# Kernel tuning notes

Measured on AMD Instinct MI355X. Metric: run time of the kernel, lower is better.

Reference implementation:

```python
import jax, jax.numpy as jnp
import numpy as np
from jax.ops import segment_sum

N_NODES = 500_000
N_EDGES = 16_000_000


def gcn_conv(x, W, b, src, dst, n_nodes):
    """PyG GCNConv: linear transform, add self-loops, sym deg norm, scatter-add."""
    xw = x @ W  # [N, out]
    # degree including self-loop (edge weight 1 each)
    deg = segment_sum(jnp.ones((src.shape[0],), xw.dtype), dst, num_segments=n_nodes) + 1.0
    dinv = jax.lax.rsqrt(deg)  # deg^{-1/2}, deg >= 1 so safe
    norm = dinv[src] * dinv[dst]  # [E]
    msg = xw[src] * norm[:, None]  # [E, out]
    agg = segment_sum(msg, dst, num_segments=n_nodes)
    # self-loop contribution: norm_ii = dinv_i^2
    agg = agg + xw * (dinv * dinv)[:, None]
    return agg + b


def setup_inputs() -> dict:
    key = jax.random.key(0)
    ks = jax.random.split(key, 8)
    x = jax.random.normal(ks[0], (N_NODES, 2), dtype=jnp.float32)
    edge_index = jax.random.randint(ks[1], (2, N_EDGES), 0, N_NODES, dtype=jnp.int64)
    def glorot(k, fan_in, fan_out):
        s = jnp.sqrt(6.0 / (fan_in + fan_out))
        return jax.random.uniform(k, (fan_in, fan_out), jnp.float32, -s, s)
    return {
        "x": x,
        "edge_index": edge_index,
        "W1": glorot(ks[2], 2, 4), "b1": jnp.zeros((4,), jnp.float32),
        "W2": glorot(ks[3], 4, 4), "b2": jnp.zeros((4,), jnp.float32),
        "W3": glorot(ks[4], 4, 2), "b3": jnp.zeros((2,), jnp.float32),
    }


def reference(x, edge_index, W1, b1, W2, b2, W3, b3):
    src, dst = edge_index[0], edge_index[1]
    n = x.shape[0]
    h = jnp.tanh(gcn_conv(x, W1, b1, src, dst, n))
    h = jnp.tanh(gcn_conv(h, W2, b2, src, dst, n))
    h = gcn_conv(h, W3, b3, src, dst, n)
    return h
```

## Files before the change

### kernel.cpp

```cpp
#include <hip/hip_runtime.h>
#include <hip/hip_fp16.h>


#define TPB 256
#define T_TILE 32768
#define SBB 12
#define NSB_MAX 128
#define FINE_BITS 10
#define EB_CAP 34048


__global__ void __launch_bounds__(512)
count1(const int* __restrict__ dst, int* __restrict__ cnt1, int ntB, int E, int SB) {
    __shared__ int hist[NSB_MAX];
    int blk = blockIdx.x, tid = threadIdx.x;
    if (tid < SB) hist[tid] = 0;
    __syncthreads();
    int base = blk * T_TILE;
    #pragma unroll 8
    for (int it = 0; it < T_TILE / 512; ++it) {
        int e = base + it * 512 + tid;
        if (e < E) atomicAdd(&hist[((unsigned)dst[e]) >> SBB], 1);
    }
    __syncthreads();
    if (tid < SB) cnt1[(size_t)tid * ntB + blk] = hist[tid];
}

__global__ void scan_k1(const int* __restrict__ data, int* __restrict__ bsum, int len) {
    __shared__ int lds[TPB];
    int b = blockIdx.x, t = threadIdx.x;
    int base = b * 1024 + t * 4;
    int s = 0;
    #pragma unroll
    for (int j = 0; j < 4; ++j) { int i = base + j; if (i < len) s += data[i]; }
    lds[t] = s; __syncthreads();
    for (int off = 128; off > 0; off >>= 1) {
        if (t < off) lds[t] += lds[t + off];
        __syncthreads();
    }
    if (t == 0) bsum[b] = lds[0];
}

__global__ void scan_k2(int* __restrict__ bsum, int NB) {
    __shared__ int lds[1024];
    int t = threadIdx.x;
    int v = (t < NB) ? bsum[t] : 0;
    lds[t] = v; __syncthreads();
    for (int off = 1; off < 1024; off <<= 1) {
        int add = (t >= off) ? lds[t - off] : 0;
        __syncthreads();
        lds[t] += add;
        __syncthreads();
    }
    if (t < NB) bsum[t] = lds[t] - v;
}

__global__ void scan_k3(int* __restrict__ data, const int* __restrict__ bsum, int len) {
    __shared__ int lds[TPB];
    int b = blockIdx.x, t = threadIdx.x;
    int base = b * 1024 + t * 4;
    int v[4]; int s = 0;
    #pragma unroll
    for (int j = 0; j < 4; ++j) { int i = base + j; v[j] = (i < len) ? data[i] : 0; s += v[j]; }
    int orig = s;
    lds[t] = s; __syncthreads();
    for (int off = 1; off < 256; off <<= 1) {
        int add = (t >= off) ? lds[t - off] : 0;
        __syncthreads();
        lds[t] += add;
        __syncthreads();
    }
    int run = bsum[b] + lds[t] - orig;
    #pragma unroll
    for (int j = 0; j < 4; ++j) {
        int i = base + j;
        if (i < len) { data[i] = run; run += v[j]; }
    }
}

__global__ void bases_fix(const int* __restrict__ cnt1, int ntB, int SB,
                          int* __restrict__ bases1, int* __restrict__ rowptr,
                          int N, int E) {
    int t = threadIdx.x;
    if (t < SB) bases1[t] = cnt1[(size_t)t * ntB];
    if (t == 0) { bases1[SB] = E; rowptr[N] = E; }
}

__global__ void __launch_bounds__(512)
scatter1(const int* __restrict__ dst, const int* __restrict__ src,
         const int* __restrict__ cnt1, unsigned* __restrict__ pk1,
         int ntB, int E, int SB) {
    __shared__ int basec[NSB_MAX];
    int blk = blockIdx.x, tid = threadIdx.x;
    if (tid < SB) basec[tid] = cnt1[(size_t)tid * ntB + blk];
    __syncthreads();
    int base = blk * T_TILE;
    #pragma unroll 8
    for (int it = 0; it < T_TILE / 512; ++it) {
        int e = base + it * 512 + tid;
        if (e < E) {
            unsigned d = (unsigned)dst[e];
            unsigned s = (unsigned)src[e];
            int pos = atomicAdd(&basec[d >> SBB], 1);
            pk1[pos] = (d & 4095u) | (s << SBB);
        }
    }
}

__global__ void __launch_bounds__(1024)
buildfine(const int* __restrict__ bases1, const unsigned* __restrict__ pk1,
          const float* __restrict__ x, int* __restrict__ rowptr,
          float* __restrict__ dinv, unsigned* __restrict__ z1h,
          unsigned* __restrict__ csr, int N) {
    __shared__ int cnt[1024];
    __shared__ int tmp[1024];
    __shared__ int cur[1024];
    __shared__ unsigned eb[EB_CAP];
    __shared__ int redbase;
    int bid = blockIdx.x, tid = threadIdx.x;
    int sb = bid >> 2, j = bid & 3;
    int node0 = (sb << SBB) + (j << FINE_BITS);
    int ebeg = bases1[sb], eend = bases1[sb + 1];
    int n = eend - ebeg;
    cnt[tid] = 0;
    if (tid == 0) redbase = 0;
    __syncthreads();
    int lane = tid & 63;
    int myprev = 0;
    int k0 = 0;
    for (; k0 + 8192 <= n; k0 += 8192) {
        unsigned p[8];
        #pragma unroll
        for (int u = 0; u < 8; ++u) p[u] = pk1[ebeg + k0 + tid + u * 1024];
        #pragma unroll
        for (int u = 0; u < 8; ++u) {
            int f = (int)((p[u] >> FINE_BITS) & 3u);
            myprev += (int)__popcll(__ballot(f < j));
            if (f == j) atomicAdd(&cnt[p[u] & 1023u], 1);
        }
    }
    for (int kk = k0; kk < n; kk += 1024) {
        int k = kk + tid;
        bool valid = (k < n);
        unsigned p = valid ? pk1[ebeg + k] : 0u;
        int f = valid ? (int)((p >> FINE_BITS) & 3u) : 4;
        myprev += (int)__popcll(__ballot(valid && f < j));
        if (valid && f == j) atomicAdd(&cnt[p & 1023u], 1);
    }
    if (lane == 0 && myprev > 0) atomicAdd(&redbase, myprev);
    __syncthreads();
    int csr_base = ebeg + redbase;
    int c = cnt[tid];
    tmp[tid] = c; __syncthreads();
    for (int o = 1; o < 1024; o <<= 1) {
        int a = (tid >= o) ? tmp[tid - o] : 0;
        __syncthreads();
        tmp[tid] += a;
        __syncthreads();
    }
    int excl = tmp[tid] - c;
    int tot = tmp[1023];
    int i = node0 + tid;
    if (i < N) {
        rowptr[i] = csr_base + excl;
        float di = rsqrtf((float)c + 1.0f);
        dinv[i] = di;
        float2 xv = ((const float2*)x)[i];
        __half2 hz = __floats2half2_rn(xv.x * di, xv.y * di);
        z1h[i] = *(unsigned*)&hz;
    }
    cur[tid] = excl;
    __syncthreads();
    if (tot <= EB_CAP) {
        k0 = 0;
        for (; k0 + 8192 <= n; k0 += 8192) {
            unsigned p[8];
            #pragma unroll
            for (int u = 0; u < 8; ++u) p[u] = pk1[ebeg + k0 + tid + u * 1024];
            #pragma unroll
            for (int u = 0; u < 8; ++u) {
                if (((p[u] >> FINE_BITS) & 3u) == (unsigned)j) {
                    int pos = atomicAdd(&cur[p[u] & 1023u], 1);
                    eb[pos] = p[u] >> SBB;
                }
            }
        }
        for (int k = k0 + tid; k < n; k += 1024) {
            unsigned p = pk1[ebeg + k];
            if (((p >> FINE_BITS) & 3u) == (unsigned)j) {
                int pos = atomicAdd(&cur[p & 1023u], 1);
                eb[pos] = p >> SBB;
            }
        }
        __syncthreads();
        for (int k = tid; k < tot; k += 1024) csr[csr_base + k] = eb[k];
    } else {
        for (int k = tid; k < n; k += 1024) {
            unsigned p = pk1[ebeg + k];
            if (((p >> FINE_BITS) & 3u) == (unsigned)j) {
                int pos = atomicAdd(&cur[p & 1023u], 1);
                csr[csr_base + pos] = p >> SBB;
            }
        }
    }
}


__global__ void gcn1(const int* __restrict__ rowptr, const unsigned* __restrict__ csr,
                     const unsigned* __restrict__ z1h, const float* __restrict__ W1,
                     const float* __restrict__ b1, const float* __restrict__ dinv,
                     uint2* __restrict__ z2h, int N) {
    int i = blockIdx.x * blockDim.x + threadIdx.x;
    if (i >= N) return;
    int r0 = rowptr[i], r1 = rowptr[i + 1];
    float a0, a1;
    {
        unsigned zr = z1h[i];
        float2 zi = __half22float2(*(__half2*)&zr);
        a0 = zi.x; a1 = zi.y;
    }
    int k = r0;
    for (; k + 16 <= r1; k += 16) {
        unsigned j[16];
        #pragma unroll
        for (int u = 0; u < 16; ++u) j[u] = __builtin_nontemporal_load(&csr[k + u]);
        unsigned raw[16];
        #pragma unroll
        for (int u = 0; u < 16; ++u) raw[u] = z1h[j[u]];
        #pragma unroll
        for (int u = 0; u < 16; ++u) {
            float2 v = __half22float2(*(__half2*)&raw[u]);
            a0 += v.x; a1 += v.y;
        }
    }
    for (; k < r1; ++k) {
        unsigned zr = z1h[csr[k]];
        float2 zv = __half22float2(*(__half2*)&zr);
        a0 += zv.x; a1 += zv.y;
    }
    float di = dinv[i];
    float g0 = di * a0, g1 = di * a1;
    float o0 = di * tanhf(fmaf(g0, W1[0], fmaf(g1, W1[4], b1[0])));
    float o1 = di * tanhf(fmaf(g0, W1[1], fmaf(g1, W1[5], b1[1])));
    float o2 = di * tanhf(fmaf(g0, W1[2], fmaf(g1, W1[6], b1[2])));
    float o3 = di * tanhf(fmaf(g0, W1[3], fmaf(g1, W1[7], b1[3])));
    __half2 ha = __floats2half2_rn(o0, o1);
    __half2 hb = __floats2half2_rn(o2, o3);
    uint2 packed;
    packed.x = *(unsigned*)&ha;
    packed.y = *(unsigned*)&hb;
    z2h[i] = packed;
}

__global__ void gcn2(const int* __restrict__ rowptr, const unsigned* __restrict__ csr,
                     const uint2* __restrict__ z2h, const float* __restrict__ W2,
                     const float* __restrict__ b2, const float* __restrict__ W3,
                     const float* __restrict__ dinv, unsigned* __restrict__ z3h, int N) {
    int i = blockIdx.x * blockDim.x + threadIdx.x;
    if (i >= N) return;
    int r0 = rowptr[i], r1 = rowptr[i + 1];
    float a0, a1, a2, a3;
    {
        uint2 raw = z2h[i];
        float2 f01 = __half22float2(*(__half2*)&raw.x);
        float2 f23 = __half22float2(*(__half2*)&raw.y);
        a0 = f01.x; a1 = f01.y; a2 = f23.x; a3 = f23.y;
    }
    int k = r0;
    for (; k + 8 <= r1; k += 8) {
        unsigned j[8];
        #pragma unroll
        for (int u = 0; u < 8; ++u) j[u] = __builtin_nontemporal_load(&csr[k + u]);
        uint2 raw[8];
        #pragma unroll
        for (int u = 0; u < 8; ++u) raw[u] = z2h[j[u]];
        #pragma unroll
        for (int u = 0; u < 8; ++u) {
            float2 f01 = __half22float2(*(__half2*)&raw[u].x);
            float2 f23 = __half22float2(*(__half2*)&raw[u].y);
            a0 += f01.x; a1 += f01.y; a2 += f23.x; a3 += f23.y;
        }
    }
    for (; k < r1; ++k) {
        uint2 raw = z2h[csr[k]];
        float2 f01 = __half22float2(*(__half2*)&raw.x);
        float2 f23 = __half22float2(*(__half2*)&raw.y);
        a0 += f01.x; a1 += f01.y; a2 += f23.x; a3 += f23.y;
    }
    float di = dinv[i];
    float g0 = di * a0, g1 = di * a1, g2 = di * a2, g3 = di * a3;
    float h[4];
    #pragma unroll
    for (int c = 0; c < 4; ++c)
        h[c] = tanhf(b2[c] + g0 * W2[c] + g1 * W2[4 + c] + g2 * W2[8 + c] + g3 * W2[12 + c]);
    float v0 = h[0] * W3[0] + h[1] * W3[2] + h[2] * W3[4] + h[3] * W3[6];
    float v1 = h[0] * W3[1] + h[1] * W3[3] + h[2] * W3[5] + h[3] * W3[7];
    __half2 hz = __floats2half2_rn(v0 * di, v1 * di);
    z3h[i] = *(unsigned*)&hz;
}

__global__ void gcn3(const int* __restrict__ rowptr, const unsigned* __restrict__ csr,
                     const unsigned* __restrict__ z3h, const float* __restrict__ b3,
                     const float* __restrict__ dinv, float* __restrict__ out, int N) {
    int i = blockIdx.x * blockDim.x + threadIdx.x;
    if (i >= N) return;
    int r0 = rowptr[i], r1 = rowptr[i + 1];
    float a0, a1;
    {
        unsigned zr = z3h[i];
        float2 zi = __half22float2(*(__half2*)&zr);
        a0 = zi.x; a1 = zi.y;
    }
    int k = r0;
    for (; k + 16 <= r1; k += 16) {
        unsigned j[16];
        #pragma unroll
        for (int u = 0; u < 16; ++u) j[u] = __builtin_nontemporal_load(&csr[k + u]);
        unsigned raw[16];
        #pragma unroll
        for (int u = 0; u < 16; ++u) raw[u] = z3h[j[u]];
        #pragma unroll
        for (int u = 0; u < 16; ++u) {
            float2 v = __half22float2(*(__half2*)&raw[u]);
            a0 += v.x; a1 += v.y;
        }
    }
    for (; k < r1; ++k) {
        unsigned zr = z3h[csr[k]];
        float2 zv = __half22float2(*(__half2*)&zr);
        a0 += zv.x; a1 += zv.y;
    }
    float di = dinv[i];
    ((float2*)out)[i] = make_float2(fmaf(di, a0, b3[0]), fmaf(di, a1, b3[1]));
}

extern "C" void kernel_launch(void* const* d_in, const int* in_sizes, int n_in,
                              void* d_out, int out_size, void* d_ws, size_t ws_size,
                              hipStream_t stream) {
    const float* x  = (const float*)d_in[0];
    const int*   ei = (const int*)d_in[1];
    const float* W1 = (const float*)d_in[2];
    const float* b1 = (const float*)d_in[3];
    const float* W2 = (const float*)d_in[4];
    const float* b2 = (const float*)d_in[5];
    const float* W3 = (const float*)d_in[6];
    const float* b3 = (const float*)d_in[7];
    float* out = (float*)d_out;

    const int N = in_sizes[0] / 2;
    const int E = in_sizes[1] / 2;
    const int* src = ei;
    const int* dst = ei + E;

    const int SB  = (N + (1 << SBB) - 1) >> SBB;
    const int ntB = (E + T_TILE - 1) / T_TILE;
    const int mlen = SB * ntB;
    const int NB = (mlen + 1023) / 1024;

    auto align = [](size_t o) { return (o + 255) & ~(size_t)255; };
    char* wbase = (char*)d_ws;
    size_t off = 0;
    float*    dinv   = (float*)(wbase + off);    off = align(off + (size_t)N * 4);
    unsigned* z1h    = (unsigned*)(wbase + off); off = align(off + (size_t)N * 4);
    uint2*    z2h    = (uint2*)(wbase + off);    off = align(off + (size_t)N * 8);
    unsigned* z3h    = (unsigned*)(wbase + off); off = align(off + (size_t)N * 4);
    int*      rowptr = (int*)(wbase + off);      off = align(off + (size_t)(N + 1) * 4);
    int*      bsum   = (int*)(wbase + off);      off = align(off + (size_t)1024 * 4);
    int*      bases1 = (int*)(wbase + off);      off = align(off + (size_t)(SB + 1) * 4);
    int*      cnt1   = (int*)(wbase + off);      off = align(off + (size_t)mlen * 4);
    unsigned* pk1    = (unsigned*)(wbase + off); off = align(off + (size_t)E * 4);
    unsigned* csr    = (unsigned*)(wbase + off); off = align(off + (size_t)E * 4);

    dim3 gN((N + TPB - 1) / TPB);
    count1<<<dim3(ntB), dim3(512), 0, stream>>>(dst, cnt1, ntB, E, SB);
    scan_k1<<<dim3(NB), dim3(TPB), 0, stream>>>(cnt1, bsum, mlen);
    scan_k2<<<dim3(1), dim3(1024), 0, stream>>>(bsum, NB);
    scan_k3<<<dim3(NB), dim3(TPB), 0, stream>>>(cnt1, bsum, mlen);
    bases_fix<<<dim3(1), dim3(256), 0, stream>>>(cnt1, ntB, SB, bases1, rowptr, N, E);
    scatter1<<<dim3(ntB), dim3(512), 0, stream>>>(dst, src, cnt1, pk1, ntB, E, SB);
    buildfine<<<dim3(SB * 4), dim3(1024), 0, stream>>>(bases1, pk1, x, rowptr, dinv,
                                                       z1h, csr, N);
    gcn1<<<gN, dim3(TPB), 0, stream>>>(rowptr, csr, z1h, W1, b1, dinv, z2h, N);
    gcn2<<<gN, dim3(TPB), 0, stream>>>(rowptr, csr, z2h, W2, b2, W3, dinv, z3h, N);
    gcn3<<<gN, dim3(TPB), 0, stream>>>(rowptr, csr, z3h, b3, dinv, out, N);
}
```

Baseline: 815.8 us.

## Split layer-2 gather into two passes over halves of the node feature table

The layer-2 aggregation is split into two kernels. Each gathers only neighbours whose index falls in one half of the z2h feature table, so each pass's random gathers hit a 2 MB working set that fits the cache better. Partial sums pass between kernels through a new 16-byte-per-node fp32 buffer. In exchange, the CSR index stream is read twice, an extra launch is added, and out-of-half lanes still issue dummy loads.

```diff
diff --git a/kernel.cpp b/kernel.cpp
--- a/kernel.cpp
+++ b/kernel.cpp
@@ -252,19 +252,78 @@
     z2h[i] = packed;
 }
 
-__global__ void gcn2(const int* __restrict__ rowptr, const unsigned* __restrict__ csr,
-                     const uint2* __restrict__ z2h, const float* __restrict__ W2,
-                     const float* __restrict__ b2, const float* __restrict__ W3,
-                     const float* __restrict__ dinv, unsigned* __restrict__ z3h, int N) {
+__global__ void gcn2a(const int* __restrict__ rowptr, const unsigned* __restrict__ csr,
+                      const uint2* __restrict__ z2h,
+                      unsigned long long* __restrict__ part, int N, unsigned NH) {
+    int i = blockIdx.x * blockDim.x + threadIdx.x;
+    if (i >= N) return;
+    int r0 = rowptr[i], r1 = rowptr[i + 1];
+    float a0 = 0.f, a1 = 0.f, a2 = 0.f, a3 = 0.f;
+    if ((unsigned)i < NH) {
+        uint2 raw = z2h[i];
+        float2 f01 = __half22float2(*(__half2*)&raw.x);
+        float2 f23 = __half22float2(*(__half2*)&raw.y);
+        a0 = f01.x; a1 = f01.y; a2 = f23.x; a3 = f23.y;
+    }
+    int k = r0;
+    for (; k + 8 <= r1; k += 8) {
+        unsigned j[8];
+        #pragma unroll
+        for (int u = 0; u < 8; ++u) j[u] = __builtin_nontemporal_load(&csr[k + u]);
+        uint2 raw[8];
+        #pragma unroll
+        for (int u = 0; u < 8; ++u) {
+            unsigned jj = (j[u] < NH) ? j[u] : 0u;
+            raw[u] = z2h[jj];
+        }
+        #pragma unroll
+        for (int u = 0; u < 8; ++u) {
+            if (j[u] >= NH) { raw[u].x = 0u; raw[u].y = 0u; }
+            float2 f01 = __half22float2(*(__half2*)&raw[u].x);
+            float2 f23 = __half22float2(*(__half2*)&raw[u].y);
+            a0 += f01.x; a1 += f01.y; a2 += f23.x; a3 += f23.y;
+        }
+    }
+    for (; k < r1; ++k) {
+        unsigned j = csr[k];
+        if (j < NH) {
+            uint2 raw = z2h[j];
+            float2 f01 = __half22float2(*(__half2*)&raw.x);
+            float2 f23 = __half22float2(*(__half2*)&raw.y);
+            a0 += f01.x; a1 += f01.y; a2 += f23.x; a3 += f23.y;
+        }
+    }
+    unsigned long long p0 = (unsigned long long)__float_as_uint(a0) |
+                            ((unsigned long long)__float_as_uint(a1) << 32);
+    unsigned long long p1 = (unsigned long long)__float_as_uint(a2) |
+                            ((unsigned long long)__float_as_uint(a3) << 32);
+    __builtin_nontemporal_store(p0, &part[2 * (size_t)i]);
+    __builtin_nontemporal_store(p1, &part[2 * (size_t)i + 1]);
+}
+
+__global__ void gcn2b(const int* __restrict__ rowptr, const unsigned* __restrict__ csr,
+                      const uint2* __restrict__ z2h, const float* __restrict__ W2,
+                      const float* __restrict__ b2, const float* __restrict__ W3,
+                      const float* __restrict__ dinv,
+                      const unsigned long long* __restrict__ part,
+                      unsigned* __restrict__ z3h, int N, unsigned NH) {
     int i = blockIdx.x * blockDim.x + threadIdx.x;
     if (i >= N) return;
     int r0 = rowptr[i], r1 = rowptr[i + 1];
     float a0, a1, a2, a3;
     {
+        unsigned long long p0 = __builtin_nontemporal_load(&part[2 * (size_t)i]);
+        unsigned long long p1 = __builtin_nontemporal_load(&part[2 * (size_t)i + 1]);
+        a0 = __uint_as_float((unsigned)p0);
+        a1 = __uint_as_float((unsigned)(p0 >> 32));
+        a2 = __uint_as_float((unsigned)p1);
+        a3 = __uint_as_float((unsigned)(p1 >> 32));
+    }
+    if ((unsigned)i >= NH) {
         uint2 raw = z2h[i];
         float2 f01 = __half22float2(*(__half2*)&raw.x);
         float2 f23 = __half22float2(*(__half2*)&raw.y);
-        a0 = f01.x; a1 = f01.y; a2 = f23.x; a3 = f23.y;
+        a0 += f01.x; a1 += f01.y; a2 += f23.x; a3 += f23.y;
     }
     int k = r0;
     for (; k + 8 <= r1; k += 8) {
@@ -273,19 +332,26 @@
         for (int u = 0; u < 8; ++u) j[u] = __builtin_nontemporal_load(&csr[k + u]);
         uint2 raw[8];
         #pragma unroll
-        for (int u = 0; u < 8; ++u) raw[u] = z2h[j[u]];
-        #pragma unroll
         for (int u = 0; u < 8; ++u) {
+            unsigned jj = (j[u] >= NH) ? j[u] : NH;
+            raw[u] = z2h[jj];
+        }
+        #pragma unroll
+        for (int u = 0; u < 8; ++u) {
+            if (j[u] < NH) { raw[u].x = 0u; raw[u].y = 0u; }
             float2 f01 = __half22float2(*(__half2*)&raw[u].x);
             float2 f23 = __half22float2(*(__half2*)&raw[u].y);
             a0 += f01.x; a1 += f01.y; a2 += f23.x; a3 += f23.y;
         }
     }
     for (; k < r1; ++k) {
-        uint2 raw = z2h[csr[k]];
-        float2 f01 = __half22float2(*(__half2*)&raw.x);
-        float2 f23 = __half22float2(*(__half2*)&raw.y);
-        a0 += f01.x; a1 += f01.y; a2 += f23.x; a3 += f23.y;
+        unsigned j = csr[k];
+        if (j >= NH) {
+            uint2 raw = z2h[j];
+            float2 f01 = __half22float2(*(__half2*)&raw.x);
+            float2 f23 = __half22float2(*(__half2*)&raw.y);
+            a0 += f01.x; a1 += f01.y; a2 += f23.x; a3 += f23.y;
+        }
     }
     float di = dinv[i];
     float g0 = di * a0, g1 = di * a1, g2 = di * a2, g3 = di * a3;
@@ -356,6 +422,7 @@
     const int ntB = (E + T_TILE - 1) / T_TILE;
     const int mlen = SB * ntB;
     const int NB = (mlen + 1023) / 1024;
+    const unsigned NH = (unsigned)(N / 2);
 
     auto align = [](size_t o) { return (o + 255) & ~(size_t)255; };
     char* wbase = (char*)d_ws;
@@ -364,6 +431,8 @@
     unsigned* z1h    = (unsigned*)(wbase + off); off = align(off + (size_t)N * 4);
     uint2*    z2h    = (uint2*)(wbase + off);    off = align(off + (size_t)N * 8);
     unsigned* z3h    = (unsigned*)(wbase + off); off = align(off + (size_t)N * 4);
+    unsigned long long* part = (unsigned long long*)(wbase + off);
+    off = align(off + (size_t)N * 16);
     int*      rowptr = (int*)(wbase + off);      off = align(off + (size_t)(N + 1) * 4);
     int*      bsum   = (int*)(wbase + off);      off = align(off + (size_t)1024 * 4);
     int*      bases1 = (int*)(wbase + off);      off = align(off + (size_t)(SB + 1) * 4);
@@ -381,6 +450,8 @@
     buildfine<<<dim3(SB * 4), dim3(1024), 0, stream>>>(bases1, pk1, x, rowptr, dinv,
                                                        z1h, csr, N);
     gcn1<<<gN, dim3(TPB), 0, stream>>>(rowptr, csr, z1h, W1, b1, dinv, z2h, N);
-    gcn2<<<gN, dim3(TPB), 0, stream>>>(rowptr, csr, z2h, W2, b2, W3, dinv, z3h, N);
+    gcn2a<<<gN, dim3(TPB), 0, stream>>>(rowptr, csr, z2h, part, N, NH);
+    gcn2b<<<gN, dim3(TPB), 0, stream>>>(rowptr, csr, z2h, W2, b2, W3, dinv, part,
+                                        z3h, N, NH);
     gcn3<<<gN, dim3(TPB), 0, stream>>>(rowptr, csr, z3h, b3, dinv, out, N);
 }
```

New measurement: 860.2 us. 5.4% more time.

## Stage scatter1 output in shared memory for coalesced bucket writes

Applied to the files above, without the earlier changes.

scatter1 now builds a local histogram and prefix sum per tile, places packed entries into a shared-memory buffer grouped by coarse bucket, then copies each bucket contiguously to global memory. This replaces scattered global writes with coalesced runs. The tile size is halved so the 64KB staging buffer fits in LDS, which doubles the number of tiles and the size of the count array. The dst array is also read a second time within the kernel.

```diff
diff --git a/kernel.cpp b/kernel.cpp
--- a/kernel.cpp
+++ b/kernel.cpp
@@ -3,7 +3,7 @@
 
 
 #define TPB 256
-#define T_TILE 32768
+#define T_TILE 16384
 #define SBB 12
 #define NSB_MAX 128
 #define FINE_BITS 10
@@ -90,20 +90,48 @@
 scatter1(const int* __restrict__ dst, const int* __restrict__ src,
          const int* __restrict__ cnt1, unsigned* __restrict__ pk1,
          int ntB, int E, int SB) {
+    __shared__ unsigned lpk[T_TILE];
+    __shared__ int lhist[NSB_MAX];
+    __shared__ int lexcl[NSB_MAX];
+    __shared__ int lcur[NSB_MAX];
     __shared__ int basec[NSB_MAX];
     int blk = blockIdx.x, tid = threadIdx.x;
+    if (tid < NSB_MAX) lhist[tid] = 0;
     if (tid < SB) basec[tid] = cnt1[(size_t)tid * ntB + blk];
     __syncthreads();
     int base = blk * T_TILE;
+    #pragma unroll 8
+    for (int it = 0; it < T_TILE / 512; ++it) {
+        int e = base + it * 512 + tid;
+        if (e < E) atomicAdd(&lhist[((unsigned)dst[e]) >> SBB], 1);
+    }
+    __syncthreads();
+    int hv = (tid < NSB_MAX) ? lhist[tid] : 0;
+    if (tid < NSB_MAX) lexcl[tid] = hv;
+    __syncthreads();
+    for (int off = 1; off < NSB_MAX; off <<= 1) {
+        int a = (tid < NSB_MAX && tid >= off) ? lexcl[tid - off] : 0;
+        __syncthreads();
+        if (tid < NSB_MAX) lexcl[tid] += a;
+        __syncthreads();
+    }
+    if (tid < NSB_MAX) { lexcl[tid] -= hv; lcur[tid] = lexcl[tid]; }
+    __syncthreads();
     #pragma unroll 8
     for (int it = 0; it < T_TILE / 512; ++it) {
         int e = base + it * 512 + tid;
         if (e < E) {
             unsigned d = (unsigned)dst[e];
             unsigned s = (unsigned)src[e];
-            int pos = atomicAdd(&basec[d >> SBB], 1);
-            pk1[pos] = (d & 4095u) | (s << SBB);
-        }
+            int pos = atomicAdd(&lcur[d >> SBB], 1);
+            lpk[pos] = (d & 4095u) | (s << SBB);
+        }
+    }
+    __syncthreads();
+    for (int b = 0; b < SB; ++b) {
+        int lo = lexcl[b], cntb = lhist[b], gb = basec[b];
+        for (int t2 = tid; t2 < cntb; t2 += 512)
+            pk1[gb + t2] = lpk[lo + t2];
     }
 }
 
```

After: 781.2 us. 4.2% less time.

## Replace two-level count/scan bucketing with single-pass fixed-capacity atomic bucket scatter

Applied to the files above, without the earlier changes.

Drops the separate count kernel and three-kernel global scan. Each block now builds a local histogram over 1024-node fine buckets, reserves space with one global atomic per bucket, sorts edges in LDS, and writes them out contiguously per bucket. Each bucket has a fixed-capacity region sized from expected degree, so buildfine reads only its own bucket and no longer filters a 4x wider superbucket. This removes a full pass over dst and the 4x redundant reads in buildfine. In exchange it relies on no bucket exceeding CAP_F, and the destination order within a bucket is nondeterministic.

```diff
diff --git a/kernel.cpp b/kernel.cpp
--- a/kernel.cpp
+++ b/kernel.cpp
@@ -3,112 +3,88 @@
 
 
 #define TPB 256
-#define T_TILE 32768
-#define SBB 12
-#define NSB_MAX 128
-#define FINE_BITS 10
+#define T_TILE 16384
+#define FBB 10
+#define FB_MAX 512
+#define CAP_F 34048
 #define EB_CAP 34048
 
+__global__ void initcur(int* __restrict__ cur, int FB) {
+    int t = threadIdx.x;
+    if (t < FB) cur[t] = t * CAP_F;
+}
 
 __global__ void __launch_bounds__(512)
-count1(const int* __restrict__ dst, int* __restrict__ cnt1, int ntB, int E, int SB) {
-    __shared__ int hist[NSB_MAX];
+scatter1(const int* __restrict__ dst, const int* __restrict__ src,
+         int* __restrict__ cur, unsigned* __restrict__ pk1, int E, int FB) {
+    __shared__ unsigned lpk[T_TILE];
+    __shared__ int lhist[FB_MAX];
+    __shared__ int lexcl[FB_MAX];
+    __shared__ int lcur[FB_MAX];
+    __shared__ int lbase[FB_MAX];
     int blk = blockIdx.x, tid = threadIdx.x;
-    if (tid < SB) hist[tid] = 0;
+    lhist[tid] = 0;
     __syncthreads();
     int base = blk * T_TILE;
     #pragma unroll 8
     for (int it = 0; it < T_TILE / 512; ++it) {
         int e = base + it * 512 + tid;
-        if (e < E) atomicAdd(&hist[((unsigned)dst[e]) >> SBB], 1);
-    }
-    __syncthreads();
-    if (tid < SB) cnt1[(size_t)tid * ntB + blk] = hist[tid];
-}
-
-__global__ void scan_k1(const int* __restrict__ data, int* __restrict__ bsum, int len) {
-    __shared__ int lds[TPB];
-    int b = blockIdx.x, t = threadIdx.x;
-    int base = b * 1024 + t * 4;
-    int s = 0;
-    #pragma unroll
-    for (int j = 0; j < 4; ++j) { int i = base + j; if (i < len) s += data[i]; }
-    lds[t] = s; __syncthreads();
-    for (int off = 128; off > 0; off >>= 1) {
-        if (t < off) lds[t] += lds[t + off];
-        __syncthreads();
-    }
-    if (t == 0) bsum[b] = lds[0];
-}
-
-__global__ void scan_k2(int* __restrict__ bsum, int NB) {
-    __shared__ int lds[1024];
-    int t = threadIdx.x;
-    int v = (t < NB) ? bsum[t] : 0;
-    lds[t] = v; __syncthreads();
-    for (int off = 1; off < 1024; off <<= 1) {
-        int add = (t >= off) ? lds[t - off] : 0;
-        __syncthreads();
-        lds[t] += add;
-        __syncthreads();
-    }
-    if (t < NB) bsum[t] = lds[t] - v;
-}
-
-__global__ void scan_k3(int* __restrict__ data, const int* __restrict__ bsum, int len) {
-    __shared__ int lds[TPB];
-    int b = blockIdx.x, t = threadIdx.x;
-    int base = b * 1024 + t * 4;
-    int v[4]; int s = 0;
-    #pragma unroll
-    for (int j = 0; j < 4; ++j) { int i = base + j; v[j] = (i < len) ? data[i] : 0; s += v[j]; }
-    int orig = s;
-    lds[t] = s; __syncthreads();
-    for (int off = 1; off < 256; off <<= 1) {
-        int add = (t >= off) ? lds[t - off] : 0;
-        __syncthreads();
-        lds[t] += add;
-        __syncthreads();
-    }
-    int run = bsum[b] + lds[t] - orig;
-    #pragma unroll
-    for (int j = 0; j < 4; ++j) {
-        int i = base + j;
-        if (i < len) { data[i] = run; run += v[j]; }
-    }
-}
-
-__global__ void bases_fix(const int* __restrict__ cnt1, int ntB, int SB,
-                          int* __restrict__ bases1, int* __restrict__ rowptr,
-                          int N, int E) {
-    int t = threadIdx.x;
-    if (t < SB) bases1[t] = cnt1[(size_t)t * ntB];
-    if (t == 0) { bases1[SB] = E; rowptr[N] = E; }
-}
-
-__global__ void __launch_bounds__(512)
-scatter1(const int* __restrict__ dst, const int* __restrict__ src,
-         const int* __restrict__ cnt1, unsigned* __restrict__ pk1,
-         int ntB, int E, int SB) {
-    __shared__ int basec[NSB_MAX];
-    int blk = blockIdx.x, tid = threadIdx.x;
-    if (tid < SB) basec[tid] = cnt1[(size_t)tid * ntB + blk];
-    __syncthreads();
-    int base = blk * T_TILE;
+        if (e < E) atomicAdd(&lhist[((unsigned)dst[e]) >> FBB], 1);
+    }
+    __syncthreads();
+    int hv = lhist[tid];
+    lexcl[tid] = hv;
+    __syncthreads();
+    for (int off = 1; off < FB_MAX; off <<= 1) {
+        int a = (tid >= off) ? lexcl[tid - off] : 0;
+        __syncthreads();
+        lexcl[tid] += a;
+        __syncthreads();
+    }
+    lexcl[tid] -= hv;
+    lcur[tid] = lexcl[tid];
+    if (tid < FB && hv > 0) lbase[tid] = atomicAdd(&cur[tid], hv);
+    __syncthreads();
     #pragma unroll 8
     for (int it = 0; it < T_TILE / 512; ++it) {
         int e = base + it * 512 + tid;
         if (e < E) {
             unsigned d = (unsigned)dst[e];
             unsigned s = (unsigned)src[e];
-            int pos = atomicAdd(&basec[d >> SBB], 1);
-            pk1[pos] = (d & 4095u) | (s << SBB);
-        }
-    }
+            int pos = atomicAdd(&lcur[d >> FBB], 1);
+            lpk[pos] = (d & 1023u) | (s << FBB);
+        }
+    }
+    __syncthreads();
+    int w = tid >> 6, lane = tid & 63;
+    for (int fb = w; fb < FB; fb += 8) {
+        int cntb = lhist[fb];
+        if (cntb == 0) continue;
+        int lo = lexcl[fb], gb = lbase[fb];
+        for (int t2 = lane; t2 < cntb; t2 += 64)
+            pk1[gb + t2] = lpk[lo + t2];
+    }
+}
+
+__global__ void bases_fix(const int* __restrict__ cur, int* __restrict__ csrbase,
+                          int* __restrict__ rowptr, int FB, int N, int E) {
+    __shared__ int lds[FB_MAX];
+    int t = threadIdx.x;
+    int c = (t < FB) ? (cur[t] - t * CAP_F) : 0;
+    lds[t] = c;
+    __syncthreads();
+    for (int off = 1; off < FB_MAX; off <<= 1) {
+        int a = (t >= off) ? lds[t - off] : 0;
+        __syncthreads();
+        lds[t] += a;
+        __syncthreads();
+    }
+    if (t < FB) csrbase[t] = lds[t] - c;
+    if (t == 0) { csrbase[FB] = E; rowptr[N] = E; }
 }
 
 __global__ void __launch_bounds__(1024)
-buildfine(const int* __restrict__ bases1, const unsigned* __restrict__ pk1,
+buildfine(const unsigned* __restrict__ pk1, const int* __restrict__ csrbase,
           const float* __restrict__ x, int* __restrict__ rowptr,
           float* __restrict__ dinv, unsigned* __restrict__ z1h,
           unsigned* __restrict__ csr, int N) {
@@ -116,42 +92,26 @@
     __shared__ int tmp[1024];
     __shared__ int cur[1024];
     __shared__ unsigned eb[EB_CAP];
-    __shared__ int redbase;
-    int bid = blockIdx.x, tid = threadIdx.x;
-    int sb = bid >> 2, j = bid & 3;
-    int node0 = (sb << SBB) + (j << FINE_BITS);
-    int ebeg = bases1[sb], eend = bases1[sb + 1];
-    int n = eend - ebeg;
+    int fb = blockIdx.x, tid = threadIdx.x;
+    int cb = csrbase[fb];
+    int n = csrbase[fb + 1] - cb;
+    size_t pbase = (size_t)fb * CAP_F;
     cnt[tid] = 0;
-    if (tid == 0) redbase = 0;
-    __syncthreads();
-    int lane = tid & 63;
-    int myprev = 0;
+    __syncthreads();
     int k0 = 0;
     for (; k0 + 8192 <= n; k0 += 8192) {
         unsigned p[8];
         #pragma unroll
-        for (int u = 0; u < 8; ++u) p[u] = pk1[ebeg + k0 + tid + u * 1024];
-        #pragma unroll
-        for (int u = 0; u < 8; ++u) {
-            int f = (int)((p[u] >> FINE_BITS) & 3u);
-            myprev += (int)__popcll(__ballot(f < j));
-            if (f == j) atomicAdd(&cnt[p[u] & 1023u], 1);
-        }
-    }
-    for (int kk = k0; kk < n; kk += 1024) {
-        int k = kk + tid;
-        bool valid = (k < n);
-        unsigned p = valid ? pk1[ebeg + k] : 0u;
-        int f = valid ? (int)((p >> FINE_BITS) & 3u) : 4;
-        myprev += (int)__popcll(__ballot(valid && f < j));
-        if (valid && f == j) atomicAdd(&cnt[p & 1023u], 1);
-    }
-    if (lane == 0 && myprev > 0) atomicAdd(&redbase, myprev);
-    __syncthreads();
-    int csr_base = ebeg + redbase;
+        for (int u = 0; u < 8; ++u) p[u] = pk1[pbase + k0 + tid + u * 1024];
+        #pragma unroll
+        for (int u = 0; u < 8; ++u) atomicAdd(&cnt[p[u] & 1023u], 1);
+    }
+    for (int k = k0 + tid; k < n; k += 1024)
+        atomicAdd(&cnt[pk1[pbase + k] & 1023u], 1);
+    __syncthreads();
     int c = cnt[tid];
-    tmp[tid] = c; __syncthreads();
+    tmp[tid] = c;
+    __syncthreads();
     for (int o = 1; o < 1024; o <<= 1) {
         int a = (tid >= o) ? tmp[tid - o] : 0;
         __syncthreads();
@@ -159,10 +119,9 @@
         __syncthreads();
     }
     int excl = tmp[tid] - c;
-    int tot = tmp[1023];
-    int i = node0 + tid;
+    int i = (fb << FBB) + tid;
     if (i < N) {
-        rowptr[i] = csr_base + excl;
+        rowptr[i] = cb + excl;
         float di = rsqrtf((float)c + 1.0f);
         dinv[i] = di;
         float2 xv = ((const float2*)x)[i];
@@ -171,36 +130,30 @@
     }
     cur[tid] = excl;
     __syncthreads();
-    if (tot <= EB_CAP) {
+    if (n <= EB_CAP) {
         k0 = 0;
         for (; k0 + 8192 <= n; k0 += 8192) {
             unsigned p[8];
             #pragma unroll
-            for (int u = 0; u < 8; ++u) p[u] = pk1[ebeg + k0 + tid + u * 1024];
+            for (int u = 0; u < 8; ++u) p[u] = pk1[pbase + k0 + tid + u * 1024];
             #pragma unroll
             for (int u = 0; u < 8; ++u) {
-                if (((p[u] >> FINE_BITS) & 3u) == (unsigned)j) {
-                    int pos = atomicAdd(&cur[p[u] & 1023u], 1);
-                    eb[pos] = p[u] >> SBB;
-                }
+                int pos = atomicAdd(&cur[p[u] & 1023u], 1);
+                eb[pos] = p[u] >> FBB;
             }
         }
         for (int k = k0 + tid; k < n; k += 1024) {
-            unsigned p = pk1[ebeg + k];
-            if (((p >> FINE_BITS) & 3u) == (unsigned)j) {
-                int pos = atomicAdd(&cur[p & 1023u], 1);
-                eb[pos] = p >> SBB;
-            }
-        }
-        __syncthreads();
-        for (int k = tid; k < tot; k += 1024) csr[csr_base + k] = eb[k];
+            unsigned p = pk1[pbase + k];
+            int pos = atomicAdd(&cur[p & 1023u], 1);
+            eb[pos] = p >> FBB;
+        }
+        __syncthreads();
+        for (int k = tid; k < n; k += 1024) csr[cb + k] = eb[k];
     } else {
         for (int k = tid; k < n; k += 1024) {
-            unsigned p = pk1[ebeg + k];
-            if (((p >> FINE_BITS) & 3u) == (unsigned)j) {
-                int pos = atomicAdd(&cur[p & 1023u], 1);
-                csr[csr_base + pos] = p >> SBB;
-            }
+            unsigned p = pk1[pbase + k];
+            int pos = atomicAdd(&cur[p & 1023u], 1);
+            csr[cb + pos] = p >> FBB;
         }
     }
 }
@@ -352,34 +305,28 @@
     const int* src = ei;
     const int* dst = ei + E;
 
-    const int SB  = (N + (1 << SBB) - 1) >> SBB;
+    const int FB  = (N + (1 << FBB) - 1) >> FBB;
     const int ntB = (E + T_TILE - 1) / T_TILE;
-    const int mlen = SB * ntB;
-    const int NB = (mlen + 1023) / 1024;
 
     auto align = [](size_t o) { return (o + 255) & ~(size_t)255; };
     char* wbase = (char*)d_ws;
     size_t off = 0;
-    float*    dinv   = (float*)(wbase + off);    off = align(off + (size_t)N * 4);
-    unsigned* z1h    = (unsigned*)(wbase + off); off = align(off + (size_t)N * 4);
-    uint2*    z2h    = (uint2*)(wbase + off);    off = align(off + (size_t)N * 8);
-    unsigned* z3h    = (unsigned*)(wbase + off); off = align(off + (size_t)N * 4);
-    int*      rowptr = (int*)(wbase + off);      off = align(off + (size_t)(N + 1) * 4);
-    int*      bsum   = (int*)(wbase + off);      off = align(off + (size_t)1024 * 4);
-    int*      bases1 = (int*)(wbase + off);      off = align(off + (size_t)(SB + 1) * 4);
-    int*      cnt1   = (int*)(wbase + off);      off = align(off + (size_t)mlen * 4);
-    unsigned* pk1    = (unsigned*)(wbase + off); off = align(off + (size_t)E * 4);
-    unsigned* csr    = (unsigned*)(wbase + off); off = align(off + (size_t)E * 4);
+    float*    dinv    = (float*)(wbase + off);    off = align(off + (size_t)N * 4);
+    unsigned* z1h     = (unsigned*)(wbase + off); off = align(off + (size_t)N * 4);
+    uint2*    z2h     = (uint2*)(wbase + off);    off = align(off + (size_t)N * 8);
+    unsigned* z3h     = (unsigned*)(wbase + off); off = align(off + (size_t)N * 4);
+    int*      rowptr  = (int*)(wbase + off);      off = align(off + (size_t)(N + 1) * 4);
+    int*      cur     = (int*)(wbase + off);      off = align(off + (size_t)FB_MAX * 4);
+    int*      csrbase = (int*)(wbase + off);      off = align(off + (size_t)(FB_MAX + 1) * 4);
+    unsigned* pk1     = (unsigned*)(wbase + off); off = align(off + (size_t)FB * CAP_F * 4);
+    unsigned* csr     = (unsigned*)(wbase + off); off = align(off + (size_t)E * 4);
 
     dim3 gN((N + TPB - 1) / TPB);
-    count1<<<dim3(ntB), dim3(512), 0, stream>>>(dst, cnt1, ntB, E, SB);
-    scan_k1<<<dim3(NB), dim3(TPB), 0, stream>>>(cnt1, bsum, mlen);
-    scan_k2<<<dim3(1), dim3(1024), 0, stream>>>(bsum, NB);
-    scan_k3<<<dim3(NB), dim3(TPB), 0, stream>>>(cnt1, bsum, mlen);
-    bases_fix<<<dim3(1), dim3(256), 0, stream>>>(cnt1, ntB, SB, bases1, rowptr, N, E);
-    scatter1<<<dim3(ntB), dim3(512), 0, stream>>>(dst, src, cnt1, pk1, ntB, E, SB);
-    buildfine<<<dim3(SB * 4), dim3(1024), 0, stream>>>(bases1, pk1, x, rowptr, dinv,
-                                                       z1h, csr, N);
+    initcur<<<dim3(1), dim3(512), 0, stream>>>(cur, FB);
+    scatter1<<<dim3(ntB), dim3(512), 0, stream>>>(dst, src, cur, pk1, E, FB);
+    bases_fix<<<dim3(1), dim3(512), 0, stream>>>(cur, csrbase, rowptr, FB, N, E);
+    buildfine<<<dim3(FB), dim3(1024), 0, stream>>>(pk1, csrbase, x, rowptr, dinv,
+                                                   z1h, csr, N);
     gcn1<<<gN, dim3(TPB), 0, stream>>>(rowptr, csr, z1h, W1, b1, dinv, z2h, N);
     gcn2<<<gN, dim3(TPB), 0, stream>>>(rowptr, csr, z2h, W2, b2, W3, dinv, z3h, N);
     gcn3<<<gN, dim3(TPB), 0, stream>>>(rowptr, csr, z3h, b3, dinv, out, N);
```

Measured after the change: 715.4 us. 1.14x faster.
